# Optimization experiments

Hardware: AMD Instinct MI355X
Metric: run time of the kernel (lower is better)

Reference implementation:

```python
import jax, jax.numpy as jnp
import numpy as np
import math

HIDDEN = 1024
HEADS = 16
HEAD_DIM = HIDDEN // HEADS
B, S = 2, 2048


def setup_inputs() -> dict:
    key = jax.random.key(0)
    ks = jax.random.split(key, 10)
    std = 1.0 / math.sqrt(HIDDEN)
    mk = lambda k: (jax.random.normal(k, (HIDDEN, HIDDEN), jnp.float32) * std)
    return {
        "hidden_states": jax.random.normal(ks[0], (B, S, HIDDEN), jnp.float32),
        "attention_mask": jnp.zeros((B, 1, 1, S), jnp.float32),
        "wq": mk(ks[1]), "bq": jnp.zeros((HIDDEN,), jnp.float32),
        "wk": mk(ks[2]), "bk": jnp.zeros((HIDDEN,), jnp.float32),
        "wv": mk(ks[3]), "bv": jnp.zeros((HIDDEN,), jnp.float32),
        "wo": mk(ks[4]), "bo": jnp.zeros((HIDDEN,), jnp.float32),
    }


def reference(hidden_states, attention_mask, wq, bq, wk, bk, wv, bv, wo, bo):
    b, s, _ = hidden_states.shape
    scale = math.sqrt(HEAD_DIM)
    # projections (torch Linear: x @ W.T + b); weights stored as [out, in]
    q = hidden_states @ wq.T + bq
    k = hidden_states @ wk.T + bk
    v = hidden_states @ wv.T + bv
    # [B, H, S, D]
    q = q.reshape(b, s, HEADS, HEAD_DIM).transpose(0, 2, 1, 3)
    k = k.reshape(b, s, HEADS, HEAD_DIM).transpose(0, 2, 1, 3)
    v = v.reshape(b, s, HEADS, HEAD_DIM).transpose(0, 2, 1, 3)
    scores = jnp.einsum("bhqd,bhkd->bhqk", q, k) / scale
    scores = scores + attention_mask  # broadcast [B,1,1,S]
    weights = jax.nn.softmax(scores, axis=-1)  # dropout = identity (eval)
    out = jnp.einsum("bhqk,bhkd->bhqd", weights, v)
    out = out.transpose(0, 2, 1, 3).reshape(b, s, HIDDEN)
    out = out @ wo.T + bo
    return out
```

## Files before the change

### kernel.cpp

```cpp
#include <hip/hip_runtime.h>
#include <hip/hip_bf16.h>

typedef __bf16 bf16_t;
typedef __bf16 bf16x8 __attribute__((ext_vector_type(8)));
typedef _Float16 f16x4 __attribute__((ext_vector_type(4)));
typedef _Float16 f16x8 __attribute__((ext_vector_type(8)));
typedef float f32x4 __attribute__((ext_vector_type(4)));

#define SEQ    2048
#define NH     16
#define HD     64
#define HIDDEN 1024
#define LOG2E  1.44269504f
#define CSTR   41

#if __has_builtin(__builtin_amdgcn_exp2f)
#define EXP2F(x) __builtin_amdgcn_exp2f(x)
#else
#define EXP2F(x) exp2f(x)
#endif

__device__ __forceinline__ bf16_t to_bf16(float f) { return (bf16_t)f; }

__device__ __forceinline__ void async16(const void* g, void* l) {
    __builtin_amdgcn_global_load_lds((const __attribute__((address_space(1))) void*)g,
                                     (__attribute__((address_space(3))) void*)l, 16, 0, 0);
}

__global__ __launch_bounds__(256) void cvt_kernel(
    const float* __restrict__ s0, bf16_t* __restrict__ d0, int c0,
    const float* __restrict__ s1, bf16_t* __restrict__ d1, int c1,
    const float* __restrict__ s2, bf16_t* __restrict__ d2, int c2,
    const float* __restrict__ s3, bf16_t* __restrict__ d3, int c3,
    const float* __restrict__ s4, bf16_t* __restrict__ d4, int c4)
{
    int blk = blockIdx.x;
    const float* s; bf16_t* d;
    if (blk < c0)              { s = s0; d = d0; }
    else if ((blk -= c0) < c1) { s = s1; d = d1; }
    else if ((blk -= c1) < c2) { s = s2; d = d2; }
    else if ((blk -= c2) < c3) { s = s3; d = d3; }
    else                       { blk -= c3; s = s4; d = d4; }
    const size_t base = (size_t)blk * 2048 + threadIdx.x * 8;
    const float4 a = *(const float4*)&s[base];
    const float4 b = *(const float4*)&s[base + 4];
    bf16x8 o;
    o[0] = (bf16_t)a.x; o[1] = (bf16_t)a.y; o[2] = (bf16_t)a.z; o[3] = (bf16_t)a.w;
    o[4] = (bf16_t)b.x; o[5] = (bf16_t)b.y; o[6] = (bf16_t)b.z; o[7] = (bf16_t)b.w;
    *(bf16x8*)&d[base] = o;
}

__global__ __launch_bounds__(256, 3) void qkv_kernel(
    const bf16_t* __restrict__ X,
    const bf16_t* __restrict__ wq, const bf16_t* __restrict__ wk, const bf16_t* __restrict__ wv,
    const float* __restrict__ bq, const float* __restrict__ bk, const float* __restrict__ bv,
    bf16_t* __restrict__ qws, bf16_t* __restrict__ kws, _Float16* __restrict__ vws)
{
    __shared__ __align__(16) bf16_t Sh[16384];
    const int z = blockIdx.z;
    const bf16_t* Wsel = (z == 0) ? wq : (z == 1) ? wk : wv;
    const float*  bsel = (z == 0) ? bq : (z == 1) ? bk : bv;
    const int m0 = blockIdx.y * 128, n0 = blockIdx.x * 128;

    const int t = threadIdx.x, lane = t & 63, w = t >> 6;
    const int w0 = w & 1, w1 = w >> 1, l15 = lane & 15, q4 = lane >> 4;

    f32x4 acc[4][4];
#pragma unroll
    for (int i = 0; i < 4; i++)
#pragma unroll
        for (int j = 0; j < 4; j++) acc[i][j] = f32x4{0.f, 0.f, 0.f, 0.f};

    auto stage = [&](int kt, int buf) {
#pragma unroll
        for (int j = 0; j < 2; j++) {
            const int s = j * 256 + t;
            const int row = s >> 2, c = (s & 3) ^ (row & 3);
            const int lb = buf * 8192 + (j * 256 + w * 64) * 8;
            async16(&X[(size_t)(m0 + row) * HIDDEN + kt + c * 8], &Sh[lb]);
            async16(&Wsel[(size_t)(n0 + row) * HIDDEN + kt + c * 8], &Sh[lb + 4096]);
        }
    };
    stage(0, 0);

    for (int it = 0; it < 32; it++) {
        const int cur = it & 1;
        __syncthreads();
        if (it < 31) stage((it + 1) * 32, cur ^ 1);
        const bf16_t* As = &Sh[cur * 8192];
        const bf16_t* Bs = &Sh[cur * 8192 + 4096];
        bf16x8 af[4];
#pragma unroll
        for (int ti = 0; ti < 4; ti++) {
            const int ra = w0 * 64 + ti * 16 + l15;
            af[ti] = *(const bf16x8*)&As[ra * 32 + (q4 ^ (ra & 3)) * 8];
        }
#pragma unroll
        for (int tj = 0; tj < 4; tj++) {
            const int rb = w1 * 64 + tj * 16 + l15;
            const bf16x8 bfr = *(const bf16x8*)&Bs[rb * 32 + (q4 ^ (rb & 3)) * 8];
#pragma unroll
            for (int ti = 0; ti < 4; ti++)
                acc[ti][tj] = __builtin_amdgcn_mfma_f32_16x16x32_bf16(af[ti], bfr, acc[ti][tj], 0, 0, 0);
        }
    }
    __syncthreads();

    if (z < 2) {
#pragma unroll
        for (int tj = 0; tj < 4; tj++) {
            const int n = w1 * 64 + tj * 16 + l15;
            const float bb = bsel[n0 + n];
            const int ch = (n >> 3), sub = n & 7;
#pragma unroll
            for (int ti = 0; ti < 4; ti++)
#pragma unroll
                for (int r = 0; r < 4; r++) {
                    const int m = w0 * 64 + ti * 16 + q4 * 4 + r;
                    Sh[m * 128 + ((ch ^ (m & 15)) << 3) + sub] = to_bf16(acc[ti][tj][r] + bb);
                }
        }
        __syncthreads();
        bf16_t* dst = (z == 0) ? qws : kws;
#pragma unroll
        for (int i = 0; i < 8; i++) {
            const int g = i * 256 + t;
            const int row = g >> 4, c = g & 15;
            const bf16x8 vv = *(const bf16x8*)&Sh[row * 128 + ((c ^ (row & 15)) << 3)];
            *(bf16x8*)&dst[(size_t)(m0 + row) * HIDDEN + n0 + c * 8] = vv;
        }
    } else {
        _Float16* Vt = (_Float16*)Sh;
#pragma unroll
        for (int tj = 0; tj < 4; tj++) {
            const int n = w1 * 64 + tj * 16 + l15;
            const float bb = bsel[n0 + n];
#pragma unroll
            for (int ti = 0; ti < 4; ti++) {
                const int mb = w0 * 64 + ti * 16 + q4 * 4;
                f16x4 v;
#pragma unroll
                for (int r = 0; r < 4; r++) v[r] = (_Float16)(acc[ti][tj][r] + bb);
                *(f16x4*)&Vt[n * 128 + (((mb >> 3) ^ (n & 15)) << 3) + (mb & 7)] = v;
            }
        }
        __syncthreads();
        const int b = m0 >> 11, sbase = m0 & (SEQ - 1);
#pragma unroll
        for (int i = 0; i < 8; i++) {
            const int g = i * 256 + t;
            const int row = g >> 4, c = g & 15;
            const f16x8 vv = *(const f16x8*)&Vt[row * 128 + ((c ^ (row & 15)) << 3)];
            const int d = (n0 + row) & 63, hh = (n0 + row) >> 6;
            *(f16x8*)&vws[(((size_t)b * NH + hh) * HD + d) * SEQ + sbase + c * 8] = vv;
        }
    }
}

__global__ __launch_bounds__(256, 2) void attn_kernel(
    const bf16_t* __restrict__ Qw, const bf16_t* __restrict__ Kw,
    const _Float16* __restrict__ Vtw, const float* __restrict__ Mask,
    bf16_t* __restrict__ Ow)
{
    __shared__ __align__(16) bf16_t Tiles[2][2][2][64 * 64];

    const int t = threadIdx.x, lane = t & 63, w = t >> 6;
    const int l15 = lane & 15, q4 = lane >> 4;
    const int wq = w & 1, kh = w >> 1;
    const int lid = blockIdx.x;
    const int c8 = lid & 7, j = lid >> 3;
    const int bh = c8 * 4 + (j >> 5);
    const int q0 = (j & 31) * 64;
    const int b = bh >> 4, h = bh & 15;

    const bf16_t* Qh = Qw + (size_t)b * SEQ * HIDDEN + h * HD;
    const bf16_t* Kh = Kw + (size_t)b * SEQ * HIDDEN + h * HD;
    const _Float16* Vh = Vtw + (size_t)bh * HD * SEQ;
    const float* Mrow = Mask + (size_t)b * SEQ;

    bf16x8 qf[2][2];
#pragma unroll
    for (int nq = 0; nq < 2; nq++)
#pragma unroll
        for (int ks = 0; ks < 2; ks++)
            qf[nq][ks] = *(const bf16x8*)&Qh[(size_t)(q0 + wq * 32 + nq * 16 + l15) * HIDDEN + ks * 32 + q4 * 8];

    f32x4 oacc[2][4];
#pragma unroll
    for (int nq = 0; nq < 2; nq++)
#pragma unroll
        for (int nb = 0; nb < 4; nb++) oacc[nq][nb] = f32x4{0.f, 0.f, 0.f, 0.f};
    float psum[2] = {0.f, 0.f};

    const int kbase = kh * (SEQ / 2);
    const int s0_ = wq * 64 + lane;

    auto stageKV = [&](int ti, int buf) {
        const int kt = kbase + ti * 64;
        bf16_t*   Kd = &Tiles[kh][buf][0][0];
        _Float16* Vd = (_Float16*)&Tiles[kh][buf][1][0];
#pragma unroll
        for (int jj = 0; jj < 4; jj++) {
            const int s = jj * 128 + s0_;
            const int row = s >> 3, c = (s & 7) ^ (row & 7);
            const int lbase = (jj * 128 + wq * 64) * 8;
            async16(&Kh[(size_t)(kt + row) * HIDDEN + c * 8], &Kd[lbase]);
            async16(&Vh[(size_t)row * SEQ + kt + c * 8], &Vd[lbase]);
        }
    };

    stageKV(0, 0);

    for (int it = 0; it < 16; it++) {
        const int cur = it & 1;
        __syncthreads();
        if (it < 15) stageKV(it + 1, cur ^ 1);

        const int kt = kbase + it * 64;
        const bf16_t*   Ksh = &Tiles[kh][cur][0][0];
        const _Float16* Vsh = (const _Float16*)&Tiles[kh][cur][1][0];

        float4 mv4[4];
#pragma unroll
        for (int cb = 0; cb < 4; cb++) mv4[cb] = *(const float4*)&Mrow[kt + cb * 16 + q4 * 4];

        f32x4 sa[2][4];
#pragma unroll
        for (int nq = 0; nq < 2; nq++)
#pragma unroll
            for (int cb = 0; cb < 4; cb++) sa[nq][cb] = f32x4{0.f, 0.f, 0.f, 0.f};
#pragma unroll
        for (int cb = 0; cb < 4; cb++)
#pragma unroll
            for (int ks = 0; ks < 2; ks++) {
                const int rk = cb * 16 + l15;
                const bf16x8 kf = *(const bf16x8*)&Ksh[rk * 64 + (((ks * 4 + q4) ^ (rk & 7))) * 8];
                sa[0][cb] = __builtin_amdgcn_mfma_f32_16x16x32_bf16(kf, qf[0][ks], sa[0][cb], 0, 0, 0);
                sa[1][cb] = __builtin_amdgcn_mfma_f32_16x16x32_bf16(kf, qf[1][ks], sa[1][cb], 0, 0, 0);
            }

        f16x4 ph[2][4];
#pragma unroll
        for (int cb = 0; cb < 4; cb++) {
            const float4 mv = mv4[cb];
            const float mk0 = mv.x * LOG2E, mk1 = mv.y * LOG2E;
            const float mk2 = mv.z * LOG2E, mk3 = mv.w * LOG2E;
#pragma unroll
            for (int nq = 0; nq < 2; nq++) {
                const float p0 = EXP2F(fmaf(sa[nq][cb][0], 0.125f * LOG2E, mk0));
                const float p1 = EXP2F(fmaf(sa[nq][cb][1], 0.125f * LOG2E, mk1));
                const float p2 = EXP2F(fmaf(sa[nq][cb][2], 0.125f * LOG2E, mk2));
                const float p3 = EXP2F(fmaf(sa[nq][cb][3], 0.125f * LOG2E, mk3));
                psum[nq] += (p0 + p1) + (p2 + p3);
                ph[nq][cb][0] = (_Float16)p0; ph[nq][cb][1] = (_Float16)p1;
                ph[nq][cb][2] = (_Float16)p2; ph[nq][cb][3] = (_Float16)p3;
            }
        }

#pragma unroll
        for (int cb = 0; cb < 4; cb++) {
#pragma unroll
            for (int nb = 0; nb < 4; nb++) {
                const int rv = nb * 16 + l15;
                const int cl = (cb * 2 + (q4 >> 1)) ^ (rv & 7);
                const f16x4 vf = *(const f16x4*)&Vsh[rv * 64 + cl * 8 + (q4 & 1) * 4];
                oacc[0][nb] = __builtin_amdgcn_mfma_f32_16x16x16f16(ph[0][cb], vf, oacc[0][nb], 0, 0, 0);
                oacc[1][nb] = __builtin_amdgcn_mfma_f32_16x16x16f16(ph[1][cb], vf, oacc[1][nb], 0, 0, 0);
            }
        }
    }
    __syncthreads();

#pragma unroll
    for (int nq = 0; nq < 2; nq++) {
        psum[nq] += __shfl_xor(psum[nq], 16);
        psum[nq] += __shfl_xor(psum[nq], 32);
    }

    float* Cb = (float*)&Tiles[0][0][0][0];
    const int crow = (wq * 64 + lane) * CSTR;
    if (kh == 1) {
#pragma unroll
        for (int nq = 0; nq < 2; nq++) {
#pragma unroll
            for (int nb = 0; nb < 4; nb++)
                *(f32x4*)&Cb[crow + (nq * 4 + nb) * 4] = oacc[nq][nb];
            Cb[crow + 32 + nq] = psum[nq];
        }
    }
    __syncthreads();
    if (kh == 0) {
#pragma unroll
        for (int nq = 0; nq < 2; nq++) {
#pragma unroll
            for (int nb = 0; nb < 4; nb++)
                oacc[nq][nb] += *(const f32x4*)&Cb[crow + (nq * 4 + nb) * 4];
            psum[nq] += Cb[crow + 32 + nq];
        }
#pragma unroll
        for (int nq = 0; nq < 2; nq++) {
            float inv[4];
#pragma unroll
            for (int r = 0; r < 4; r++) inv[r] = 1.f / __shfl(psum[nq], q4 * 4 + r);
#pragma unroll
            for (int r = 0; r < 4; r++) {
                const int s = q0 + wq * 32 + nq * 16 + q4 * 4 + r;
#pragma unroll
                for (int nb = 0; nb < 4; nb++)
                    Ow[((size_t)b * SEQ + s) * HIDDEN + h * HD + nb * 16 + l15] =
                        to_bf16(oacc[nq][nb][r] * inv[r]);
            }
        }
    }
}

__global__ __launch_bounds__(256, 2) void oproj_kernel(
    const bf16_t* __restrict__ A, const bf16_t* __restrict__ Wo,
    const float* __restrict__ bo, float* __restrict__ Out)
{
    __shared__ __align__(16) bf16_t Sh[12288];
    const int m0 = blockIdx.y * 64, n0 = blockIdx.x * 128;
    const int t = threadIdx.x, lane = t & 63, w = t >> 6;
    const int l15 = lane & 15, q4 = lane >> 4;

    f32x4 acc[4][2];
#pragma unroll
    for (int i = 0; i < 4; i++)
#pragma unroll
        for (int j = 0; j < 2; j++) acc[i][j] = f32x4{0.f, 0.f, 0.f, 0.f};

    auto stage = [&](int kt, int buf) {
        {
            const int row = t >> 2, c = (t & 3) ^ (row & 3);
            async16(&A[(size_t)(m0 + row) * HIDDEN + kt + c * 8], &Sh[buf * 6144 + w * 64 * 8]);
        }
#pragma unroll
        for (int j = 0; j < 2; j++) {
            const int s = j * 256 + t;
            const int row = s >> 2, c = (s & 3) ^ (row & 3);
            async16(&Wo[(size_t)(n0 + row) * HIDDEN + kt + c * 8],
                    &Sh[buf * 6144 + 2048 + (j * 256 + w * 64) * 8]);
        }
    };
    stage(0, 0);

    for (int it = 0; it < 32; it++) {
        const int cur = it & 1;
        __syncthreads();
        if (it < 31) stage((it + 1) * 32, cur ^ 1);
        const bf16_t* As = &Sh[cur * 6144];
        const bf16_t* Bs = &Sh[cur * 6144 + 2048];
        bf16x8 af[4];
#pragma unroll
        for (int ti = 0; ti < 4; ti++) {
            const int ra = ti * 16 + l15;
            af[ti] = *(const bf16x8*)&As[ra * 32 + (q4 ^ (ra & 3)) * 8];
        }
#pragma unroll
        for (int tj = 0; tj < 2; tj++) {
            const int rb = w * 32 + tj * 16 + l15;
            const bf16x8 bfr = *(const bf16x8*)&Bs[rb * 32 + (q4 ^ (rb & 3)) * 8];
#pragma unroll
            for (int ti = 0; ti < 4; ti++)
                acc[ti][tj] = __builtin_amdgcn_mfma_f32_16x16x32_bf16(bfr, af[ti], acc[ti][tj], 0, 0, 0);
        }
    }

#pragma unroll
    for (int tj = 0; tj < 2; tj++) {
        const int nb4 = n0 + w * 32 + tj * 16 + q4 * 4;
        const float4 bb = *(const float4*)&bo[nb4];
#pragma unroll
        for (int ti = 0; ti < 4; ti++) {
            const int m = m0 + ti * 16 + l15;
            float4 ov;
            ov.x = acc[ti][tj][0] + bb.x;
            ov.y = acc[ti][tj][1] + bb.y;
            ov.z = acc[ti][tj][2] + bb.z;
            ov.w = acc[ti][tj][3] + bb.w;
            *(float4*)&Out[(size_t)m * HIDDEN + nb4] = ov;
        }
    }
}

extern "C" void kernel_launch(void* const* d_in, const int* in_sizes, int n_in,
                              void* d_out, int out_size, void* d_ws, size_t ws_size,
                              hipStream_t stream) {
    const float* X   = (const float*)d_in[0];
    const float* msk = (const float*)d_in[1];
    const float* wq  = (const float*)d_in[2];
    const float* bq  = (const float*)d_in[3];
    const float* wk  = (const float*)d_in[4];
    const float* bk  = (const float*)d_in[5];
    const float* wv  = (const float*)d_in[6];
    const float* bv  = (const float*)d_in[7];
    const float* wo  = (const float*)d_in[8];
    const float* bo  = (const float*)d_in[9];
    float* out = (float*)d_out;

    const size_t NELT = (size_t)2 * SEQ * HIDDEN;
    const size_t WELT = (size_t)HIDDEN * HIDDEN;
    bf16_t*    xbf = (bf16_t*)d_ws;
    bf16_t*    qws = xbf + NELT;
    bf16_t*    kws = qws + NELT;
    _Float16*  vws = (_Float16*)(kws + NELT);
    bf16_t*    aws = xbf;
    bf16_t*    wqb = (bf16_t*)d_out;
    bf16_t*    wkb = wqb + WELT;
    bf16_t*    wvb = wkb + WELT;
    bf16_t*    wob = wvb + WELT;

    cvt_kernel<<<dim3(2048 + 4 * 512), dim3(256), 0, stream>>>(
        X, xbf, 2048, wq, wqb, 512, wk, wkb, 512, wv, wvb, 512, wo, wob, 512);
    qkv_kernel<<<dim3(8, 32, 3), dim3(256), 0, stream>>>(
        xbf, wqb, wkb, wvb, bq, bk, bv, qws, kws, vws);
    attn_kernel<<<dim3(1024), dim3(256), 0, stream>>>(qws, kws, vws, msk, aws);
    oproj_kernel<<<dim3(8, 64), dim3(256), 0, stream>>>(aws, wob, bo, out);
}
```

Before: 201.7 us.

## Restructure attention: one 16-row query strip per wave, drop split-K merge

The attention kernel no longer splits the key range across two wave pairs. Each of the four waves now owns 16 query rows and walks all 32 key tiles, so the LDS reduction and the extra barriers at the end go away. Shared memory is halved and launch bounds rise to 4 blocks per CU to raise occupancy. The PV product switches to 16x16x32 f16 MFMA with P packed into f16x8. In exchange each wave does half the MFMA work per K/V tile it loads, so LDS reads per FLOP rise and the serial loop is twice as long.

```diff
diff --git a/kernel.cpp b/kernel.cpp
--- a/kernel.cpp
+++ b/kernel.cpp
@@ -12,7 +12,6 @@
 #define HD     64
 #define HIDDEN 1024
 #define LOG2E  1.44269504f
-#define CSTR   41
 
 #if __has_builtin(__builtin_amdgcn_exp2f)
 #define EXP2F(x) __builtin_amdgcn_exp2f(x)
@@ -157,20 +156,19 @@
     }
 }
 
-__global__ __launch_bounds__(256, 2) void attn_kernel(
+__global__ __launch_bounds__(256, 4) void attn_kernel(
     const bf16_t* __restrict__ Qw, const bf16_t* __restrict__ Kw,
     const _Float16* __restrict__ Vtw, const float* __restrict__ Mask,
     bf16_t* __restrict__ Ow)
 {
-    __shared__ __align__(16) bf16_t Tiles[2][2][2][64 * 64];
+    __shared__ __align__(16) bf16_t Tiles[2][2][64 * 64];
 
     const int t = threadIdx.x, lane = t & 63, w = t >> 6;
     const int l15 = lane & 15, q4 = lane >> 4;
-    const int wq = w & 1, kh = w >> 1;
     const int lid = blockIdx.x;
-    const int c8 = lid & 7, j = lid >> 3;
-    const int bh = c8 * 4 + (j >> 5);
-    const int q0 = (j & 31) * 64;
+    const int c8 = lid & 7, jx = lid >> 3;
+    const int bh = c8 * 4 + (jx >> 5);
+    const int q0 = (jx & 31) * 64;
     const int b = bh >> 4, h = bh & 15;
 
     const bf16_t* Qh = Qw + (size_t)b * SEQ * HIDDEN + h * HD;
@@ -178,32 +176,26 @@
     const _Float16* Vh = Vtw + (size_t)bh * HD * SEQ;
     const float* Mrow = Mask + (size_t)b * SEQ;
 
-    bf16x8 qf[2][2];
-#pragma unroll
-    for (int nq = 0; nq < 2; nq++)
-#pragma unroll
-        for (int ks = 0; ks < 2; ks++)
-            qf[nq][ks] = *(const bf16x8*)&Qh[(size_t)(q0 + wq * 32 + nq * 16 + l15) * HIDDEN + ks * 32 + q4 * 8];
-
-    f32x4 oacc[2][4];
-#pragma unroll
-    for (int nq = 0; nq < 2; nq++)
-#pragma unroll
-        for (int nb = 0; nb < 4; nb++) oacc[nq][nb] = f32x4{0.f, 0.f, 0.f, 0.f};
-    float psum[2] = {0.f, 0.f};
-
-    const int kbase = kh * (SEQ / 2);
-    const int s0_ = wq * 64 + lane;
+    const int qrow = q0 + w * 16 + l15;
+    bf16x8 qf[2];
+#pragma unroll
+    for (int ks = 0; ks < 2; ks++)
+        qf[ks] = *(const bf16x8*)&Qh[(size_t)qrow * HIDDEN + ks * 32 + q4 * 8];
+
+    f32x4 oacc[4];
+#pragma unroll
+    for (int nb = 0; nb < 4; nb++) oacc[nb] = f32x4{0.f, 0.f, 0.f, 0.f};
+    float psum = 0.f;
 
     auto stageKV = [&](int ti, int buf) {
-        const int kt = kbase + ti * 64;
-        bf16_t*   Kd = &Tiles[kh][buf][0][0];
-        _Float16* Vd = (_Float16*)&Tiles[kh][buf][1][0];
-#pragma unroll
-        for (int jj = 0; jj < 4; jj++) {
-            const int s = jj * 128 + s0_;
+        const int kt = ti * 64;
+        bf16_t*   Kd = &Tiles[buf][0][0];
+        _Float16* Vd = (_Float16*)&Tiles[buf][1][0];
+#pragma unroll
+        for (int g = 0; g < 2; g++) {
+            const int s = g * 256 + t;
             const int row = s >> 3, c = (s & 7) ^ (row & 7);
-            const int lbase = (jj * 128 + wq * 64) * 8;
+            const int lbase = (g * 256 + w * 64) * 8;
             async16(&Kh[(size_t)(kt + row) * HIDDEN + c * 8], &Kd[lbase]);
             async16(&Vh[(size_t)row * SEQ + kt + c * 8], &Vd[lbase]);
         }
@@ -211,106 +203,75 @@
 
     stageKV(0, 0);
 
-    for (int it = 0; it < 16; it++) {
+    for (int it = 0; it < 32; it++) {
         const int cur = it & 1;
         __syncthreads();
-        if (it < 15) stageKV(it + 1, cur ^ 1);
-
-        const int kt = kbase + it * 64;
-        const bf16_t*   Ksh = &Tiles[kh][cur][0][0];
-        const _Float16* Vsh = (const _Float16*)&Tiles[kh][cur][1][0];
+        if (it < 31) stageKV(it + 1, cur ^ 1);
+
+        const int kt = it * 64;
+        const bf16_t*   Ksh = &Tiles[cur][0][0];
+        const _Float16* Vsh = (const _Float16*)&Tiles[cur][1][0];
 
         float4 mv4[4];
 #pragma unroll
         for (int cb = 0; cb < 4; cb++) mv4[cb] = *(const float4*)&Mrow[kt + cb * 16 + q4 * 4];
 
-        f32x4 sa[2][4];
-#pragma unroll
-        for (int nq = 0; nq < 2; nq++)
-#pragma unroll
-            for (int cb = 0; cb < 4; cb++) sa[nq][cb] = f32x4{0.f, 0.f, 0.f, 0.f};
-#pragma unroll
-        for (int cb = 0; cb < 4; cb++)
+        f32x4 sa[4];
+#pragma unroll
+        for (int cb = 0; cb < 4; cb++) sa[cb] = f32x4{0.f, 0.f, 0.f, 0.f};
+#pragma unroll
+        for (int cb = 0; cb < 4; cb++) {
+            const int rk = cb * 16 + l15;
 #pragma unroll
             for (int ks = 0; ks < 2; ks++) {
-                const int rk = cb * 16 + l15;
                 const bf16x8 kf = *(const bf16x8*)&Ksh[rk * 64 + (((ks * 4 + q4) ^ (rk & 7))) * 8];
-                sa[0][cb] = __builtin_amdgcn_mfma_f32_16x16x32_bf16(kf, qf[0][ks], sa[0][cb], 0, 0, 0);
-                sa[1][cb] = __builtin_amdgcn_mfma_f32_16x16x32_bf16(kf, qf[1][ks], sa[1][cb], 0, 0, 0);
+                sa[cb] = __builtin_amdgcn_mfma_f32_16x16x32_bf16(kf, qf[ks], sa[cb], 0, 0, 0);
             }
-
-        f16x4 ph[2][4];
+        }
+
+        f16x8 pa[2];
 #pragma unroll
         for (int cb = 0; cb < 4; cb++) {
             const float4 mv = mv4[cb];
-            const float mk0 = mv.x * LOG2E, mk1 = mv.y * LOG2E;
-            const float mk2 = mv.z * LOG2E, mk3 = mv.w * LOG2E;
-#pragma unroll
-            for (int nq = 0; nq < 2; nq++) {
-                const float p0 = EXP2F(fmaf(sa[nq][cb][0], 0.125f * LOG2E, mk0));
-                const float p1 = EXP2F(fmaf(sa[nq][cb][1], 0.125f * LOG2E, mk1));
-                const float p2 = EXP2F(fmaf(sa[nq][cb][2], 0.125f * LOG2E, mk2));
-                const float p3 = EXP2F(fmaf(sa[nq][cb][3], 0.125f * LOG2E, mk3));
-                psum[nq] += (p0 + p1) + (p2 + p3);
-                ph[nq][cb][0] = (_Float16)p0; ph[nq][cb][1] = (_Float16)p1;
-                ph[nq][cb][2] = (_Float16)p2; ph[nq][cb][3] = (_Float16)p3;
+            const float mk[4] = {mv.x * LOG2E, mv.y * LOG2E, mv.z * LOG2E, mv.w * LOG2E};
+#pragma unroll
+            for (int r = 0; r < 4; r++) {
+                const float p = EXP2F(fmaf(sa[cb][r], 0.125f * LOG2E, mk[r]));
+                psum += p;
+                pa[cb >> 1][(cb & 1) * 4 + r] = (_Float16)p;
             }
         }
 
 #pragma unroll
-        for (int cb = 0; cb < 4; cb++) {
+        for (int t2 = 0; t2 < 2; t2++) {
 #pragma unroll
             for (int nb = 0; nb < 4; nb++) {
                 const int rv = nb * 16 + l15;
-                const int cl = (cb * 2 + (q4 >> 1)) ^ (rv & 7);
-                const f16x4 vf = *(const f16x4*)&Vsh[rv * 64 + cl * 8 + (q4 & 1) * 4];
-                oacc[0][nb] = __builtin_amdgcn_mfma_f32_16x16x16f16(ph[0][cb], vf, oacc[0][nb], 0, 0, 0);
-                oacc[1][nb] = __builtin_amdgcn_mfma_f32_16x16x16f16(ph[1][cb], vf, oacc[1][nb], 0, 0, 0);
+                const int glo = (t2 * 4 + (q4 >> 1)) ^ (rv & 7);
+                const int ghi = (t2 * 4 + 2 + (q4 >> 1)) ^ (rv & 7);
+                const f16x4 vlo = *(const f16x4*)&Vsh[rv * 64 + (glo << 3) + (q4 & 1) * 4];
+                const f16x4 vhi = *(const f16x4*)&Vsh[rv * 64 + (ghi << 3) + (q4 & 1) * 4];
+                f16x8 vf;
+                vf[0] = vlo[0]; vf[1] = vlo[1]; vf[2] = vlo[2]; vf[3] = vlo[3];
+                vf[4] = vhi[0]; vf[5] = vhi[1]; vf[6] = vhi[2]; vf[7] = vhi[3];
+                oacc[nb] = __builtin_amdgcn_mfma_f32_16x16x32_f16(pa[t2], vf, oacc[nb], 0, 0, 0);
             }
         }
     }
-    __syncthreads();
-
-#pragma unroll
-    for (int nq = 0; nq < 2; nq++) {
-        psum[nq] += __shfl_xor(psum[nq], 16);
-        psum[nq] += __shfl_xor(psum[nq], 32);
-    }
-
-    float* Cb = (float*)&Tiles[0][0][0][0];
-    const int crow = (wq * 64 + lane) * CSTR;
-    if (kh == 1) {
-#pragma unroll
-        for (int nq = 0; nq < 2; nq++) {
-#pragma unroll
-            for (int nb = 0; nb < 4; nb++)
-                *(f32x4*)&Cb[crow + (nq * 4 + nb) * 4] = oacc[nq][nb];
-            Cb[crow + 32 + nq] = psum[nq];
-        }
-    }
-    __syncthreads();
-    if (kh == 0) {
-#pragma unroll
-        for (int nq = 0; nq < 2; nq++) {
-#pragma unroll
-            for (int nb = 0; nb < 4; nb++)
-                oacc[nq][nb] += *(const f32x4*)&Cb[crow + (nq * 4 + nb) * 4];
-            psum[nq] += Cb[crow + 32 + nq];
-        }
-#pragma unroll
-        for (int nq = 0; nq < 2; nq++) {
-            float inv[4];
-#pragma unroll
-            for (int r = 0; r < 4; r++) inv[r] = 1.f / __shfl(psum[nq], q4 * 4 + r);
-#pragma unroll
-            for (int r = 0; r < 4; r++) {
-                const int s = q0 + wq * 32 + nq * 16 + q4 * 4 + r;
-#pragma unroll
-                for (int nb = 0; nb < 4; nb++)
-                    Ow[((size_t)b * SEQ + s) * HIDDEN + h * HD + nb * 16 + l15] =
-                        to_bf16(oacc[nq][nb][r] * inv[r]);
-            }
-        }
+
+    psum += __shfl_xor(psum, 16);
+    psum += __shfl_xor(psum, 32);
+
+    float inv[4];
+#pragma unroll
+    for (int r = 0; r < 4; r++) inv[r] = 1.f / __shfl(psum, q4 * 4 + r);
+#pragma unroll
+    for (int r = 0; r < 4; r++) {
+        const int srow = q0 + w * 16 + q4 * 4 + r;
+#pragma unroll
+        for (int nb = 0; nb < 4; nb++)
+            Ow[((size_t)b * SEQ + srow) * HIDDEN + h * HD + nb * 16 + l15] =
+                to_bf16(oacc[nb][r] * inv[r]);
     }
 }
 
```

After: 200.1 us. Within noise of the previous version (-0.8%).
